# Kernel optimization log

Hardware: AMD Instinct MI355X
Metric: run time of the kernel (lower is better)

Reference implementation:

```python
import jax, jax.numpy as jnp
import numpy as np

EMBED_DIM = 1024
NUM_HEADS = 16
HEAD_DIM = EMBED_DIM // NUM_HEADS


def setup_inputs() -> dict:
    key = jax.random.key(0)
    ks = jax.random.split(key, 9)
    B, S, E = 2, 2048, EMBED_DIM
    scale = 1.0 / np.sqrt(E)
    inp = {
        "x": jax.random.normal(ks[0], (B, S, E), dtype=jnp.float32),
        "Wq": jax.random.normal(ks[1], (E, E), dtype=jnp.float32) * scale,
        "bq": jnp.zeros((E,), dtype=jnp.float32),
        "Wk": jax.random.normal(ks[2], (E, E), dtype=jnp.float32) * scale,
        "bk": jnp.zeros((E,), dtype=jnp.float32),
        "Wv": jax.random.normal(ks[3], (E, E), dtype=jnp.float32) * scale,
        "bv": jnp.zeros((E,), dtype=jnp.float32),
        "Wo": jax.random.normal(ks[4], (E, E), dtype=jnp.float32) * scale,
        "bo": jnp.zeros((E,), dtype=jnp.float32),
    }
    return inp


def reference(x, Wq, bq, Wk, bk, Wv, bv, Wo, bo):
    B, S, E = x.shape
    H, D = NUM_HEADS, HEAD_DIM
    sm_scale = D ** (-0.5)

    def proj(W, b):
        # torch Linear: x @ W.T + b ; reshape to [B, H, S, D]
        y = jnp.einsum("bse,fe->bsf", x, W) + b
        return y.reshape(B, S, H, D).transpose(0, 2, 1, 3)

    q = proj(Wq, bq)  # [B, H, S, D]
    k = proj(Wk, bk)
    v = proj(Wv, bv)

    scores = jnp.einsum("bhqd,bhkd->bhqk", q, k) * sm_scale  # [B, H, S, S]
    attn = jax.nn.softmax(scores, axis=-1)
    o = jnp.einsum("bhqk,bhkd->bhqd", attn, v)  # [B, H, S, D]
    o = o.transpose(0, 2, 1, 3).reshape(B, S, E)
    return jnp.einsum("bse,fe->bsf", o, Wo) + bo
```

## Files before the change

kernel.cpp:

```cpp
#include <hip/hip_runtime.h>
#include <hip/hip_fp16.h>
#include <stdint.h>


typedef _Float16 f16;
typedef _Float16 f16x8 __attribute__((ext_vector_type(8)));
typedef _Float16 f16x4v __attribute__((ext_vector_type(4)));
typedef float f32x4 __attribute__((ext_vector_type(4)));
typedef int i32x4 __attribute__((ext_vector_type(4)));

#define BQ  2
#define SEQ 2048
#define EMB 1024
#define NH  16
#define HD  64
#define MM  (BQ * SEQ)

__device__ __forceinline__ void gld_lds16(const void* g, void* l) {
  __builtin_amdgcn_global_load_lds(
      (const __attribute__((address_space(1))) void*)g,
      (__attribute__((address_space(3))) void*)l, 16, 0, 0);
}

__device__ __forceinline__ void stage128x64(const f16* __restrict__ src,
                                            int ld, f16* lds, int tid) {
#pragma unroll
  for (int it = 0; it < 4; ++it) {
    int idx = it * 256 + tid;
    int r = idx >> 3, c = idx & 7;
    int sc = c ^ (r & 7);
    gld_lds16(src + (size_t)r * ld + sc * 8, lds + idx * 8);
  }
}

__device__ __forceinline__ f16x8 pack8(float a0, float a1, float a2, float a3,
                                       float b0, float b1, float b2, float b3) {
  i32x4 w;
  w.x = __builtin_bit_cast(int, __builtin_amdgcn_cvt_pkrtz(a0, a1));
  w.y = __builtin_bit_cast(int, __builtin_amdgcn_cvt_pkrtz(a2, a3));
  w.z = __builtin_bit_cast(int, __builtin_amdgcn_cvt_pkrtz(b0, b1));
  w.w = __builtin_bit_cast(int, __builtin_amdgcn_cvt_pkrtz(b2, b3));
  return __builtin_bit_cast(f16x8, w);
}

__global__ void cvtAll(const float* __restrict__ x, const float* __restrict__ w0,
                       const float* __restrict__ w1, const float* __restrict__ w2,
                       const float* __restrict__ w3, f16* __restrict__ dst) {
  int i = blockIdx.x * blockDim.x + threadIdx.x;
  const float* s;
  int off;
  if (i < (1 << 20)) {
    s = x; off = i;
  } else {
    int j = i - (1 << 20);
    int w = j >> 18, o = j & ((1 << 18) - 1);
    s = (w == 0) ? w0 : (w == 1) ? w1 : (w == 2) ? w2 : w3;
    off = o;
  }
  float4 v = ((const float4*)s)[off];
  f16x4v out;
  out[0] = (f16)v.x; out[1] = (f16)v.y; out[2] = (f16)v.z; out[3] = (f16)v.w;
  ((f16x4v*)dst)[i] = out;
}

template <int MODE>
__global__ __launch_bounds__(256, 2) void gemm_bt(
    const f16* __restrict__ A, const f16* __restrict__ W0,
    const f16* __restrict__ W1, const f16* __restrict__ W2,
    const float* __restrict__ b0, const float* __restrict__ b1,
    const float* __restrict__ b2, f16* __restrict__ o0, f16* __restrict__ o1,
    f16* __restrict__ o2, float* __restrict__ fo) {
  __shared__ __align__(16) f16 As[128 * 64];
  __shared__ __align__(16) f16 Bs[128 * 64];

  const int tid = threadIdx.x, lane = tid & 63, wid = tid >> 6;
  const int o = blockIdx.x;
  const int cx = o & 7, j = o >> 3;
  const int bx = 4 * cx + (j & 3);
  int by, z;
  if (MODE == 0) { int yz = j >> 2; by = yz & 7; z = yz >> 3; }
  else           { by = j >> 2; z = 0; }
  const f16* W = (z == 0) ? W0 : (z == 1 ? W1 : W2);
  const float* bia = (z == 0) ? b0 : (z == 1 ? b1 : b2);
  f16* outp = (z == 0) ? o0 : (z == 1 ? o1 : o2);
  const int row0 = bx * 128, col0 = by * 128;
  const int wr = (wid >> 1) * 64, wc = (wid & 1) * 64;
  const int rb = lane & 15, gq = lane >> 4, sw = lane & 7;

  f32x4 acc[4][4] = {};

  for (int kt = 0; kt < EMB / 64; ++kt) {
    __syncthreads();
    stage128x64(A + (size_t)row0 * EMB + kt * 64, EMB, As, tid);
    stage128x64(W + (size_t)col0 * EMB + kt * 64, EMB, Bs, tid);
    asm volatile("s_waitcnt vmcnt(0)" ::: "memory");
    __syncthreads();
#pragma unroll
    for (int kk = 0; kk < 2; ++kk) {
      f16x8 av[4], bv[4];
#pragma unroll
      for (int f = 0; f < 4; ++f) {
        av[f] = *(const f16x8*)(As + (wr + f * 16 + rb) * 64 +
                                (((kk * 4 + gq) ^ sw) << 3));
        bv[f] = *(const f16x8*)(Bs + (wc + f * 16 + rb) * 64 +
                                (((kk * 4 + gq) ^ sw) << 3));
      }
#pragma unroll
      for (int fi = 0; fi < 4; ++fi)
#pragma unroll
        for (int fj = 0; fj < 4; ++fj)
          acc[fi][fj] = __builtin_amdgcn_mfma_f32_16x16x32_f16(
              av[fi], bv[fj], acc[fi][fj], 0, 0, 0);
    }
  }

  float bias[4];
#pragma unroll
  for (int fj = 0; fj < 4; ++fj) bias[fj] = bia[col0 + wc + fj * 16 + rb];
  const float scale = (MODE == 0 && z == 0) ? 0.18033688011112042f : 1.0f;
#pragma unroll
  for (int fi = 0; fi < 4; ++fi) {
#pragma unroll
    for (int i = 0; i < 4; ++i) {
      int row = row0 + wr + fi * 16 + gq * 4 + i;
#pragma unroll
      for (int fj = 0; fj < 4; ++fj) {
        int col = col0 + wc + fj * 16 + rb;
        float v = (acc[fi][fj][i] + bias[fj]) * scale;
        if (MODE == 0) {
          int bb = row >> 11, s = row & (SEQ - 1);
          int h = col >> 6, d = col & 63;
          outp[(((size_t)(bb * NH + h)) * SEQ + s) * HD + d] = (f16)v;
        } else {
          fo[(size_t)row * EMB + col] = v;
        }
      }
    }
  }
}

__global__ __launch_bounds__(256) void vtrans(const f16* __restrict__ V,
                                              f16* __restrict__ Vt) {
  __shared__ f16 T[64][72];
  const int tid = threadIdx.x;
  const int s0 = blockIdx.x * 64, bh = blockIdx.y;
  const f16* Vh = V + (size_t)bh * SEQ * HD;
  f16* Vth = Vt + (size_t)bh * HD * SEQ;
#pragma unroll
  for (int it = 0; it < 2; ++it) {
    int idx = it * 256 + tid;
    int r = idx >> 3, c0 = (idx & 7) * 8;
    *(f16x8*)&T[r][c0] = *(const f16x8*)(Vh + (size_t)(s0 + r) * HD + c0);
  }
  __syncthreads();
#pragma unroll
  for (int it = 0; it < 2; ++it) {
    int idx = it * 256 + tid;
    int d = idx >> 3, a = idx & 7;
    f16x8 v;
#pragma unroll
    for (int j = 0; j < 8; ++j) v[j] = T[a * 8 + j][d];
    const int base = ((a >> 2) << 5) + ((a & 1) << 4) + (((a >> 1) & 1) << 2);
    f16* dst = Vth + (size_t)d * SEQ + s0 + base;
    f16x4v w0, w1;
#pragma unroll
    for (int j = 0; j < 4; ++j) { w0[j] = v[j]; w1[j] = v[4 + j]; }
    *(f16x4v*)dst = w0;
    *(f16x4v*)(dst + 8) = w1;
  }
}

__global__ __launch_bounds__(256, 2) void attn_fwd(const f16* __restrict__ Q,
                                                   const f16* __restrict__ K,
                                                   const f16* __restrict__ Vt,
                                                   f16* __restrict__ O) {
  __shared__ __align__(16) f16 Ks[2][2][64 * 64];
  __shared__ __align__(16) f16 Vs[2][2][64 * 64];

  const int tid = threadIdx.x, lane = tid & 63;
  const int wid = tid >> 6;
  const int orig = blockIdx.x;
  const int swz = ((orig & 7) << 6) + (orig >> 3);
  const int qt = swz & 15, bh = swz >> 4;
  const f16* Qh = Q + (size_t)bh * SEQ * HD;
  const f16* Kh = K + (size_t)bh * SEQ * HD;
  const f16* Vth = Vt + (size_t)bh * HD * SEQ;
  const int q0 = qt * 128 + wid * 32;
  const int rb = lane & 15, gq = lane >> 4, sw = lane & 7;

  f16x8 aq[2][2];
#pragma unroll
  for (int qf = 0; qf < 2; ++qf)
#pragma unroll
    for (int kk = 0; kk < 2; ++kk)
      aq[qf][kk] = *(const f16x8*)(Qh + (size_t)(q0 + qf * 16 + rb) * HD +
                                   kk * 32 + gq * 8);
  asm volatile("s_waitcnt vmcnt(0)" ::: "memory");

  const int srow = tid >> 3, scol = (tid & 7) ^ (srow & 7);
  const f16* Kg0 = Kh + (size_t)srow * HD + scol * 8;
  const f16* Vg0 = Vth + (size_t)srow * SEQ + scol * 8;

  const int NT2 = SEQ / 128;
#pragma unroll
  for (int sub = 0; sub < 2; ++sub) {
    const f16* kg = Kg0 + (size_t)sub * 64 * HD;
    const f16* vg = Vg0 + sub * 64;
    gld_lds16(kg,            &Ks[0][sub][tid * 8]);
    gld_lds16(kg + 32 * HD,  &Ks[0][sub][(tid + 256) * 8]);
    gld_lds16(vg,            &Vs[0][sub][tid * 8]);
    gld_lds16(vg + 32 * SEQ, &Vs[0][sub][(tid + 256) * 8]);
  }

  f32x4 oaccA[2][4] = {};
  f32x4 oaccB[2][4] = {};
  float lsum[2] = {0.f, 0.f};

  for (int t = 0; t < NT2; ++t) {
    __builtin_amdgcn_s_barrier();
    __builtin_amdgcn_sched_barrier(0);
    {
      const int tp = (t + 1 < NT2) ? t + 1 : NT2 - 1;
      const int ns = (t + 1) & 1;
#pragma unroll
      for (int sub = 0; sub < 2; ++sub) {
        const f16* kg = Kg0 + (size_t)(2 * tp + sub) * 64 * HD;
        const f16* vg = Vg0 + (2 * tp + sub) * 64;
        gld_lds16(kg,            &Ks[ns][sub][tid * 8]);
        gld_lds16(kg + 32 * HD,  &Ks[ns][sub][(tid + 256) * 8]);
        gld_lds16(vg,            &Vs[ns][sub][tid * 8]);
        gld_lds16(vg + 32 * SEQ, &Vs[ns][sub][(tid + 256) * 8]);
      }
      asm volatile("s_waitcnt vmcnt(8)" ::: "memory");
    }
    __builtin_amdgcn_s_barrier();
    __builtin_amdgcn_sched_barrier(0);

    const int cs = t & 1;
    const f16* Kb0 = &Ks[cs][0][0];
    const f16* Kb1 = &Ks[cs][1][0];
    const f16* Vb0 = &Vs[cs][0][0];
    const f16* Vb1 = &Vs[cs][1][0];

    __builtin_amdgcn_s_setprio(1);

    f32x4 s0_[2][4] = {};
#pragma unroll
    for (int kk = 0; kk < 2; ++kk) {
      f16x8 bk[4];
#pragma unroll
      for (int cf = 0; cf < 4; ++cf)
        bk[cf] = *(const f16x8*)(Kb0 + (cf * 16 + rb) * 64 +
                                 (((kk * 4 + gq) ^ sw) << 3));
#pragma unroll
      for (int qf = 0; qf < 2; ++qf)
#pragma unroll
        for (int cf = 0; cf < 4; ++cf)
          s0_[qf][cf] = __builtin_amdgcn_mfma_f32_16x16x32_f16(
              bk[cf], aq[qf][kk], s0_[qf][cf], 0, 0, 0);
    }

    f16x8 bp0[2][2];
#pragma unroll
    for (int qf = 0; qf < 2; ++qf)
#pragma unroll
      for (int g = 0; g < 2; ++g) {
        float e0 = __builtin_amdgcn_exp2f(s0_[qf][2 * g][0]);
        float e1 = __builtin_amdgcn_exp2f(s0_[qf][2 * g][1]);
        float e2 = __builtin_amdgcn_exp2f(s0_[qf][2 * g][2]);
        float e3 = __builtin_amdgcn_exp2f(s0_[qf][2 * g][3]);
        float f0 = __builtin_amdgcn_exp2f(s0_[qf][2 * g + 1][0]);
        float f1 = __builtin_amdgcn_exp2f(s0_[qf][2 * g + 1][1]);
        float f2 = __builtin_amdgcn_exp2f(s0_[qf][2 * g + 1][2]);
        float f3 = __builtin_amdgcn_exp2f(s0_[qf][2 * g + 1][3]);
        lsum[qf] += ((e0 + e1) + (e2 + e3)) + ((f0 + f1) + (f2 + f3));
        bp0[qf][g] = pack8(e0, e1, e2, e3, f0, f1, f2, f3);
      }

    f32x4 s1_[2][4] = {};
#pragma unroll
    for (int kk = 0; kk < 2; ++kk) {
      f16x8 bk[4];
#pragma unroll
      for (int cf = 0; cf < 4; ++cf)
        bk[cf] = *(const f16x8*)(Kb1 + (cf * 16 + rb) * 64 +
                                 (((kk * 4 + gq) ^ sw) << 3));
#pragma unroll
      for (int qf = 0; qf < 2; ++qf)
#pragma unroll
        for (int cf = 0; cf < 4; ++cf)
          s1_[qf][cf] = __builtin_amdgcn_mfma_f32_16x16x32_f16(
              bk[cf], aq[qf][kk], s1_[qf][cf], 0, 0, 0);
    }

#pragma unroll
    for (int g = 0; g < 2; ++g)
#pragma unroll
      for (int df = 0; df < 4; ++df) {
        f16x8 vb = *(const f16x8*)(Vb0 + (df * 16 + rb) * 64 +
                                   (((g * 4 + gq) ^ sw) << 3));
        oaccA[0][df] = __builtin_amdgcn_mfma_f32_16x16x32_f16(
            bp0[0][g], vb, oaccA[0][df], 0, 0, 0);
        oaccA[1][df] = __builtin_amdgcn_mfma_f32_16x16x32_f16(
            bp0[1][g], vb, oaccA[1][df], 0, 0, 0);
      }

    f16x8 bp1[2][2];
#pragma unroll
    for (int qf = 0; qf < 2; ++qf)
#pragma unroll
      for (int g = 0; g < 2; ++g) {
        float e0 = __builtin_amdgcn_exp2f(s1_[qf][2 * g][0]);
        float e1 = __builtin_amdgcn_exp2f(s1_[qf][2 * g][1]);
        float e2 = __builtin_amdgcn_exp2f(s1_[qf][2 * g][2]);
        float e3 = __builtin_amdgcn_exp2f(s1_[qf][2 * g][3]);
        float f0 = __builtin_amdgcn_exp2f(s1_[qf][2 * g + 1][0]);
        float f1 = __builtin_amdgcn_exp2f(s1_[qf][2 * g + 1][1]);
        float f2 = __builtin_amdgcn_exp2f(s1_[qf][2 * g + 1][2]);
        float f3 = __builtin_amdgcn_exp2f(s1_[qf][2 * g + 1][3]);
        lsum[qf] += ((e0 + e1) + (e2 + e3)) + ((f0 + f1) + (f2 + f3));
        bp1[qf][g] = pack8(e0, e1, e2, e3, f0, f1, f2, f3);
      }

#pragma unroll
    for (int g = 0; g < 2; ++g)
#pragma unroll
      for (int df = 0; df < 4; ++df) {
        f16x8 vb = *(const f16x8*)(Vb1 + (df * 16 + rb) * 64 +
                                   (((g * 4 + gq) ^ sw) << 3));
        oaccB[0][df] = __builtin_amdgcn_mfma_f32_16x16x32_f16(
            bp1[0][g], vb, oaccB[0][df], 0, 0, 0);
        oaccB[1][df] = __builtin_amdgcn_mfma_f32_16x16x32_f16(
            bp1[1][g], vb, oaccB[1][df], 0, 0, 0);
      }

    __builtin_amdgcn_s_setprio(0);
  }
  asm volatile("s_waitcnt vmcnt(0)" ::: "memory");

  float lv[2];
#pragma unroll
  for (int qf = 0; qf < 2; ++qf) {
    float l = lsum[qf];
    l += __shfl_xor(l, 16, 64);
    l += __shfl_xor(l, 32, 64);
    lv[qf] = l;
  }

  const int b = bh >> 4, h = bh & 15;
#pragma unroll
  for (int qf = 0; qf < 2; ++qf)
#pragma unroll
    for (int i = 0; i < 4; ++i) {
      const int rsel = (gq * 4 + i) & 15;
      const float l = __shfl(lv[qf], (lane & 48) + rsel, 64);
      const float inv = 1.0f / l;
      const int s = q0 + qf * 16 + gq * 4 + i;
      f16* orow = O + ((size_t)(b * SEQ + s)) * EMB + h * 64 + rb;
#pragma unroll
      for (int df = 0; df < 4; ++df)
        orow[df * 16] =
            (f16)((oaccA[qf][df][i] + oaccB[qf][df][i]) * inv);
    }
}

extern "C" void kernel_launch(void* const* d_in, const int* in_sizes, int n_in,
                              void* d_out, int out_size, void* d_ws,
                              size_t ws_size, hipStream_t stream) {
  const float* x = (const float*)d_in[0];
  const float* Wq = (const float*)d_in[1];
  const float* bq = (const float*)d_in[2];
  const float* Wk = (const float*)d_in[3];
  const float* bk = (const float*)d_in[4];
  const float* Wv = (const float*)d_in[5];
  const float* bv = (const float*)d_in[6];
  const float* Wo = (const float*)d_in[7];
  const float* bo = (const float*)d_in[8];
  float* out = (float*)d_out;

  const size_t NX = (size_t)MM * EMB;
  const size_t NW = (size_t)EMB * EMB;

  f16* xh  = (f16*)d_ws;
  f16* wqh = xh + NX;
  f16* wkh = wqh + NW;
  f16* wvh = wkh + NW;
  f16* woh = wvh + NW;
  f16* Qw  = woh + NW;
  f16* Kw  = Qw + NX;
  f16* Vw  = Kw + NX;
  f16* Vtw = Vw + NX;
  f16* Ow  = Vtw + NX;

  cvtAll<<<dim3(8192), 256, 0, stream>>>(x, Wq, Wk, Wv, Wo, xh);

  gemm_bt<0><<<dim3(768), 256, 0, stream>>>(
      xh, wqh, wkh, wvh, bq, bk, bv, Qw, Kw, Vw, nullptr);

  vtrans<<<dim3(SEQ / 64, BQ * NH), 256, 0, stream>>>(Vw, Vtw);

  attn_fwd<<<dim3(512), 256, 0, stream>>>(Qw, Kw, Vtw, Ow);

  gemm_bt<1><<<dim3(256), 256, 0, stream>>>(
      Ow, woh, woh, woh, bo, bo, bo, nullptr, nullptr, nullptr, out);
}
```

Baseline: 104.2 us.

## Triple-buffer GEMM K-tiles with async global-to-LDS prefetch two steps ahead

Replaces the single-buffered 64-wide K loop in the projection GEMM with a 32-wide K step and a three-slot LDS ring. Each slot packs the A and W half-tiles side by side. Loads for tile kt+2 are issued before computing tile kt, and a partial vmcnt wait is used so global-to-LDS transfers overlap MFMA work. This trades twice as many barriers per K and a larger LDS footprint, which may reduce occupancy, for latency hiding.

```diff
diff --git a/kernel.cpp b/kernel.cpp
--- a/kernel.cpp
+++ b/kernel.cpp
@@ -20,17 +20,6 @@
   __builtin_amdgcn_global_load_lds(
       (const __attribute__((address_space(1))) void*)g,
       (__attribute__((address_space(3))) void*)l, 16, 0, 0);
-}
-
-__device__ __forceinline__ void stage128x64(const f16* __restrict__ src,
-                                            int ld, f16* lds, int tid) {
-#pragma unroll
-  for (int it = 0; it < 4; ++it) {
-    int idx = it * 256 + tid;
-    int r = idx >> 3, c = idx & 7;
-    int sc = c ^ (r & 7);
-    gld_lds16(src + (size_t)r * ld + sc * 8, lds + idx * 8);
-  }
 }
 
 __device__ __forceinline__ f16x8 pack8(float a0, float a1, float a2, float a3,
@@ -70,8 +59,7 @@
     const float* __restrict__ b0, const float* __restrict__ b1,
     const float* __restrict__ b2, f16* __restrict__ o0, f16* __restrict__ o1,
     f16* __restrict__ o2, float* __restrict__ fo) {
-  __shared__ __align__(16) f16 As[128 * 64];
-  __shared__ __align__(16) f16 Bs[128 * 64];
+  __shared__ __align__(16) f16 Ts[3][128 * 64];
 
   const int tid = threadIdx.x, lane = tid & 63, wid = tid >> 6;
   const int o = blockIdx.x;
@@ -87,32 +75,56 @@
   const int wr = (wid >> 1) * 64, wc = (wid & 1) * 64;
   const int rb = lane & 15, gq = lane >> 4, sw = lane & 7;
 
+  const f16* srcb[4];
+  int dsti[4];
+#pragma unroll
+  for (int it = 0; it < 4; ++it) {
+    int idx = it * 256 + tid;
+    int r = idx >> 3, c = idx & 7, sc = c ^ (r & 7);
+    srcb[it] = (sc < 4) ? A + (size_t)(row0 + r) * EMB + sc * 8
+                        : W + (size_t)(col0 + r) * EMB + (sc - 4) * 8;
+    dsti[it] = idx * 8;
+  }
+
   f32x4 acc[4][4] = {};
-
-  for (int kt = 0; kt < EMB / 64; ++kt) {
-    __syncthreads();
-    stage128x64(A + (size_t)row0 * EMB + kt * 64, EMB, As, tid);
-    stage128x64(W + (size_t)col0 * EMB + kt * 64, EMB, Bs, tid);
-    asm volatile("s_waitcnt vmcnt(0)" ::: "memory");
-    __syncthreads();
-#pragma unroll
-    for (int kk = 0; kk < 2; ++kk) {
-      f16x8 av[4], bv[4];
-#pragma unroll
-      for (int f = 0; f < 4; ++f) {
-        av[f] = *(const f16x8*)(As + (wr + f * 16 + rb) * 64 +
-                                (((kk * 4 + gq) ^ sw) << 3));
-        bv[f] = *(const f16x8*)(Bs + (wc + f * 16 + rb) * 64 +
-                                (((kk * 4 + gq) ^ sw) << 3));
-      }
-#pragma unroll
-      for (int fi = 0; fi < 4; ++fi)
-#pragma unroll
-        for (int fj = 0; fj < 4; ++fj)
-          acc[fi][fj] = __builtin_amdgcn_mfma_f32_16x16x32_f16(
-              av[fi], bv[fj], acc[fi][fj], 0, 0, 0);
-    }
-  }
+  const int NTK = EMB / 32;
+
+#pragma unroll
+  for (int p = 0; p < 2; ++p)
+#pragma unroll
+    for (int it = 0; it < 4; ++it)
+      gld_lds16(srcb[it] + p * 32, &Ts[p][dsti[it]]);
+
+  for (int kt = 0; kt < NTK; ++kt) {
+    __builtin_amdgcn_s_barrier();
+    __builtin_amdgcn_sched_barrier(0);
+    {
+      const int tp = (kt + 2 < NTK) ? kt + 2 : NTK - 1;
+      f16* Td = &Ts[(kt + 2) % 3][0];
+#pragma unroll
+      for (int it = 0; it < 4; ++it)
+        gld_lds16(srcb[it] + tp * 32, Td + dsti[it]);
+      asm volatile("s_waitcnt vmcnt(8)" ::: "memory");
+    }
+    __builtin_amdgcn_s_barrier();
+    __builtin_amdgcn_sched_barrier(0);
+
+    const f16* Tb = &Ts[kt % 3][0];
+    f16x8 av[4], bv[4];
+#pragma unroll
+    for (int f = 0; f < 4; ++f) {
+      av[f] = *(const f16x8*)(Tb + (wr + f * 16 + rb) * 64 + ((gq ^ sw) << 3));
+      bv[f] = *(const f16x8*)(Tb + (wc + f * 16 + rb) * 64 +
+                              (((4 + gq) ^ sw) << 3));
+    }
+#pragma unroll
+    for (int fi = 0; fi < 4; ++fi)
+#pragma unroll
+      for (int fj = 0; fj < 4; ++fj)
+        acc[fi][fj] = __builtin_amdgcn_mfma_f32_16x16x32_f16(
+            av[fi], bv[fj], acc[fi][fj], 0, 0, 0);
+  }
+  asm volatile("s_waitcnt vmcnt(0)" ::: "memory");
 
   float bias[4];
 #pragma unroll
```

Result: slower. 107.7 us (+3.4%).
